# Performance work log

Hardware: AMD Instinct MI355X
Metric: run time of the kernel (lower is better)

The kernel has to match this reference:

```python
import jax, jax.numpy as jnp
import numpy as np

N = 50000       # nodes
E = 800000      # edges (avg degree 16)
IN = 256        # in_features
HEAD = 4        # attention heads (conv1/conv2 out_channels)
F_OUT = 32      # mlp output features per head


def setup_inputs() -> dict:
    key = jax.random.key(0)
    ks = jax.random.split(key, 6)
    feat = jax.random.normal(ks[0], (N, IN), dtype=jnp.float32)
    edge_index = jax.random.randint(ks[1], (2, E), 0, N, dtype=jnp.int64)
    s = 1.0 / np.sqrt(IN)
    # mlp: Linear(IN -> HEAD*F_OUT)
    W_mlp = jax.random.uniform(ks[2], (IN, HEAD * F_OUT), jnp.float32, -s, s)
    b_mlp = jnp.zeros((HEAD * F_OUT,), jnp.float32)
    # conv1/conv2: 1x1 Conv1d(IN -> HEAD) == linear projection
    W1 = jax.random.uniform(ks[3], (HEAD, IN), jnp.float32, -s, s)
    b1 = jnp.zeros((HEAD,), jnp.float32)
    W2 = jax.random.uniform(ks[4], (HEAD, IN), jnp.float32, -s, s)
    b2 = jnp.zeros((HEAD,), jnp.float32)
    eps = jnp.zeros((1,), jnp.float32)  # trainable eps, init 0
    return {"feat": feat, "edge_index": edge_index, "W_mlp": W_mlp,
            "b_mlp": b_mlp, "W1": W1, "b1": b1, "W2": W2, "b2": b2,
            "eps": eps}


def reference(feat, edge_index, W_mlp, b_mlp, W1, b1, W2, b2, eps):
    n = feat.shape[0]
    head = W1.shape[0]
    # mlp: [N, IN] -> [N, head*F] -> [head, N, F]
    x = (feat @ W_mlp + b_mlp).reshape(n, head, -1).transpose(1, 0, 2)
    # 1x1 conv projections -> per-node attention logits [head, N]
    h1 = (feat @ W1.T + b1).T
    h2 = (feat @ W2.T + b2).T
    src = edge_index[0]  # edge[0]
    dst = edge_index[1]  # edge[1]
    # per-edge attention value, relu (dropout=0 -> identity): [head, E]
    v = jax.nn.relu(h1[:, src] + h2[:, dst])
    # gather neighbor features and weight: [head, E, F]
    msg = x[:, dst, :] * v[:, :, None]
    # scatter-add into destination nodes indexed by src: [N, head, F]
    agg = jax.ops.segment_sum(msg.transpose(1, 0, 2), src, num_segments=n)
    h_prime = agg.transpose(1, 0, 2) + eps[0] * x   # [head, N, F]
    # permute(1,0,2).reshape(N, -1) -> [N, head*F]
    return h_prime.transpose(1, 0, 2).reshape(n, -1)
```

## Files before the change

### kernel.cpp

```cpp
#include <hip/hip_runtime.h>

#define NN   50000
#define EE   800000
#define INF  256
#define COUT 128
#define BTROWS 144
#define PROJ_BLOCKS 782
#define CAP  52

typedef __attribute__((ext_vector_type(8))) short short8;
typedef __attribute__((ext_vector_type(4))) float f32x4;

__device__ __forceinline__ float b2f(unsigned short u) {
    union { unsigned int i; float f; } c;
    c.i = ((unsigned int)u) << 16;
    return c.f;
}
__device__ __forceinline__ unsigned short f2b(float f) {
    union { float f; unsigned int i; } c;
    c.f = f;
    unsigned int i = c.i;
    unsigned int lsb = (i >> 16) & 1u;
    i += 0x7fffu + lsb;
    return (unsigned short)(i >> 16);
}

__global__ __launch_bounds__(256) void zero_bt_kernel(
    const float* __restrict__ Wm, const float* __restrict__ W1,
    const float* __restrict__ W2,
    unsigned short* __restrict__ BT, int* __restrict__ cursor)
{
    const int t = threadIdx.x;
    if (blockIdx.x < 49) {
        const int idx = blockIdx.x * 256 + t;
        if (idx < 12500) ((int4*)cursor)[idx] = make_int4(0, 0, 0, 0);
    } else {
        const int n = blockIdx.x - 49;
        const int k = t;
        float v;
        if      (n < 128) v = Wm[k * COUT + n];
        else if (n < 132) v = W1[(n - 128) * INF + k];
        else if (n < 136) v = W2[(n - 132) * INF + k];
        else              v = 0.f;
        BT[n * INF + k] = f2b(v);
    }
}

#define LSTRIDE 72
__global__ __launch_bounds__(256) void proj_scatter_kernel(
    const float* __restrict__ feat,
    const unsigned short* __restrict__ BT,
    const float* __restrict__ bm,
    const float* __restrict__ b1,
    const float* __restrict__ b2,
    unsigned short* __restrict__ x_out,
    unsigned short* __restrict__ hh,
    const int* __restrict__ edge,
    int* __restrict__ cursor,
    unsigned short* __restrict__ sdst)
{
    __shared__ short lA[64 * LSTRIDE];
    __shared__ short lB[BTROWS * LSTRIDE];

    const int t = threadIdx.x;

    if (blockIdx.x >= PROJ_BLOCKS) {
        const int e = (blockIdx.x - PROJ_BLOCKS) * 256 + t;
        const int s = edge[e];
        const int d = edge[EE + e];
        const int p = atomicAdd(&cursor[s], 1);
        if (p < CAP) sdst[s * CAP + p] = (unsigned short)d;
        return;
    }

    const int lane  = t & 63;
    const int wave  = t >> 6;
    const int quad  = lane >> 4;
    const int col   = lane & 15;
    const int node0 = blockIdx.x * 64;

    f32x4 acc[9];
    #pragma unroll
    for (int i = 0; i < 9; i++) acc[i] = (f32x4){0.f, 0.f, 0.f, 0.f};

    for (int kc = 0; kc < 4; kc++) {
        const int k0 = kc * 64;
        #pragma unroll
        for (int p = 0; p < 4; p++) {
            const int idx = p * 256 + t;
            const int row = idx >> 4;
            const int c4  = idx & 15;
            const int grow = node0 + row;
            float4 f = make_float4(0.f, 0.f, 0.f, 0.f);
            if (grow < NN) f = *(const float4*)(feat + grow * INF + k0 + c4 * 4);
            short4 s;
            s.x = (short)f2b(f.x); s.y = (short)f2b(f.y);
            s.z = (short)f2b(f.z); s.w = (short)f2b(f.w);
            *(short4*)&lA[row * LSTRIDE + c4 * 4] = s;
        }
        #pragma unroll
        for (int p = 0; p < 5; p++) {
            const int idx = p * 256 + t;
            if (idx < (BTROWS * 64) / 8) {
                const int row = idx >> 3;
                const int c8  = idx & 7;
                uint4 u = *(const uint4*)(BT + row * INF + k0 + c8 * 8);
                *(uint4*)&lB[row * LSTRIDE + c8 * 8] = u;
            }
        }
        __syncthreads();

        #pragma unroll
        for (int ks = 0; ks < 2; ks++) {
            short8 a = *(const short8*)&lA[(wave * 16 + col) * LSTRIDE + ks * 32 + quad * 8];
            #pragma unroll
            for (int nt = 0; nt < 9; nt++) {
                short8 b = *(const short8*)&lB[(nt * 16 + col) * LSTRIDE + ks * 32 + quad * 8];
                acc[nt] = __builtin_amdgcn_mfma_f32_16x16x32_bf16(a, b, acc[nt], 0, 0, 0);
            }
        }
        __syncthreads();
    }

    const int rbase = node0 + wave * 16 + quad * 4;
    #pragma unroll
    for (int nt = 0; nt < 8; nt++) {
        const float bias = bm[nt * 16 + col];
        #pragma unroll
        for (int r = 0; r < 4; r++) {
            const int row = rbase + r;
            if (row < NN) x_out[row * COUT + nt * 16 + col] = f2b(acc[nt][r] + bias);
        }
    }
    if (col < 8) {
        const float bias = (col < 4) ? b1[col] : b2[col - 4];
        #pragma unroll
        for (int r = 0; r < 4; r++) {
            const int row = rbase + r;
            if (row < NN) hh[row * 8 + col] = f2b(acc[8][r] + bias);
        }
    }
}

__global__ __launch_bounds__(256) void accum_kernel(
    const int* __restrict__ cursor,
    const unsigned short* __restrict__ sdst,
    const unsigned short* __restrict__ x,
    const unsigned short* __restrict__ hh,
    const float* __restrict__ eps,
    float* __restrict__ out)
{
    const int lane = threadIdx.x & 63;
    const int node = blockIdx.x * 4 + (threadIdx.x >> 6);
    if (node >= NN) return;

    const int sub = lane & 7;
    const int g   = lane >> 3;
    const int h   = sub >> 1;

    const int deg = min(cursor[node], CAP);

    ushort4 h1u = *(const ushort4*)(hh + node * 8);

    int dv = 0;
    unsigned int vv01 = 0, vv23 = 0;
    if (lane < deg) {
        dv = (int)sdst[node * CAP + lane];
        ushort4 h2u = *(const ushort4*)(hh + dv * 8 + 4);
        const float v0 = b2f(h1u.x) + b2f(h2u.x);
        const float v1 = b2f(h1u.y) + b2f(h2u.y);
        const float v2 = b2f(h1u.z) + b2f(h2u.z);
        const float v3 = b2f(h1u.w) + b2f(h2u.w);
        vv01 = (unsigned int)f2b(v0) | ((unsigned int)f2b(v1) << 16);
        vv23 = (unsigned int)f2b(v2) | ((unsigned int)f2b(v3) << 16);
    }

    float acc[16];
    #pragma unroll
    for (int r = 0; r < 16; r++) acc[r] = 0.f;

    for (int i0 = 0; i0 < deg; i0 += 8) {
        const int idx = i0 + g;
        const int d = __shfl(dv, idx);
        const unsigned int u01 = (unsigned int)__shfl((int)vv01, idx);
        const unsigned int u23 = (unsigned int)__shfl((int)vv23, idx);
        unsigned short vb;
        if      (h == 0) vb = (unsigned short)(u01 & 0xffffu);
        else if (h == 1) vb = (unsigned short)(u01 >> 16);
        else if (h == 2) vb = (unsigned short)(u23 & 0xffffu);
        else             vb = (unsigned short)(u23 >> 16);
        const float v = b2f(vb);
        if (idx < deg && v > 0.f) {
            const unsigned short* xr = x + d * COUT + sub * 16;
            uint4 u0 = *(const uint4*)(xr);
            uint4 u1 = *(const uint4*)(xr + 8);
            acc[0]  = fmaf(b2f((unsigned short)(u0.x & 0xffffu)), v, acc[0]);
            acc[1]  = fmaf(b2f((unsigned short)(u0.x >> 16)),     v, acc[1]);
            acc[2]  = fmaf(b2f((unsigned short)(u0.y & 0xffffu)), v, acc[2]);
            acc[3]  = fmaf(b2f((unsigned short)(u0.y >> 16)),     v, acc[3]);
            acc[4]  = fmaf(b2f((unsigned short)(u0.z & 0xffffu)), v, acc[4]);
            acc[5]  = fmaf(b2f((unsigned short)(u0.z >> 16)),     v, acc[5]);
            acc[6]  = fmaf(b2f((unsigned short)(u0.w & 0xffffu)), v, acc[6]);
            acc[7]  = fmaf(b2f((unsigned short)(u0.w >> 16)),     v, acc[7]);
            acc[8]  = fmaf(b2f((unsigned short)(u1.x & 0xffffu)), v, acc[8]);
            acc[9]  = fmaf(b2f((unsigned short)(u1.x >> 16)),     v, acc[9]);
            acc[10] = fmaf(b2f((unsigned short)(u1.y & 0xffffu)), v, acc[10]);
            acc[11] = fmaf(b2f((unsigned short)(u1.y >> 16)),     v, acc[11]);
            acc[12] = fmaf(b2f((unsigned short)(u1.z & 0xffffu)), v, acc[12]);
            acc[13] = fmaf(b2f((unsigned short)(u1.z >> 16)),     v, acc[13]);
            acc[14] = fmaf(b2f((unsigned short)(u1.w & 0xffffu)), v, acc[14]);
            acc[15] = fmaf(b2f((unsigned short)(u1.w >> 16)),     v, acc[15]);
        }
    }

    #pragma unroll
    for (int r = 0; r < 16; r++) {
        acc[r] += __shfl_xor(acc[r], 8);
        acc[r] += __shfl_xor(acc[r], 16);
        acc[r] += __shfl_xor(acc[r], 32);
    }

    if (lane < 8) {
        const float e = eps[0];
        const unsigned short* xr = x + node * COUT + sub * 16;
        uint4 u0 = *(const uint4*)(xr);
        uint4 u1 = *(const uint4*)(xr + 8);
        unsigned int uu[8] = {u0.x, u0.y, u0.z, u0.w, u1.x, u1.y, u1.z, u1.w};
        #pragma unroll
        for (int q = 0; q < 8; q++) {
            acc[2 * q]     = fmaf(e, b2f((unsigned short)(uu[q] & 0xffffu)), acc[2 * q]);
            acc[2 * q + 1] = fmaf(e, b2f((unsigned short)(uu[q] >> 16)),     acc[2 * q + 1]);
        }
        float* o = out + node * COUT + sub * 16;
        #pragma unroll
        for (int q = 0; q < 4; q++)
            *(float4*)(o + q * 4) = make_float4(acc[4 * q], acc[4 * q + 1],
                                                acc[4 * q + 2], acc[4 * q + 3]);
    }
}

extern "C" void kernel_launch(void* const* d_in, const int* in_sizes, int n_in,
                              void* d_out, int out_size, void* d_ws, size_t ws_size,
                              hipStream_t stream) {
    const float* feat = (const float*)d_in[0];
    const int*   edge = (const int*)d_in[1];
    const float* Wm   = (const float*)d_in[2];
    const float* bm   = (const float*)d_in[3];
    const float* W1   = (const float*)d_in[4];
    const float* b1   = (const float*)d_in[5];
    const float* W2   = (const float*)d_in[6];
    const float* b2   = (const float*)d_in[7];
    const float* eps  = (const float*)d_in[8];

    char* ws = (char*)d_ws;
    unsigned short* x      = (unsigned short*)ws;
    unsigned short* hh     = (unsigned short*)(ws + 12800000);
    int*            cursor = (int*)(ws + 13600000);
    unsigned short* sdst   = (unsigned short*)(ws + 13800000);
    unsigned short* BT     = (unsigned short*)d_out;

    zero_bt_kernel<<<193, 256, 0, stream>>>(Wm, W1, W2, BT, cursor);
    proj_scatter_kernel<<<PROJ_BLOCKS + 3125, 256, 0, stream>>>(
        feat, BT, bm, b1, b2, x, hh, edge, cursor, sdst);
    accum_kernel<<<(NN + 3) / 4, 256, 0, stream>>>(cursor, sdst, x, hh, eps,
                                                   (float*)d_out);
}
```

Measured before the change: 189.1 us.

## Replace per-node global atomics with two-level bucketed adjacency build in LDS

Edge scatter now bins edges into 196 buckets of 256 source nodes, using block-local LDS histograms and one global atomic per bucket per block instead of one global atomic per edge. A new kernel then builds each bucket's fixed-capacity adjacency lists in shared memory and writes them out as coalesced 8-byte stores along with the per-node counts. This is meant to cut global atomic contention and scattered 2-byte writes, at the cost of an extra kernel launch, an intermediate packed buffer placed in the output scratch area, and a per-bucket capacity limit of 4608 that could drop edges if a bucket overflows.

```diff
diff --git a/kernel.cpp b/kernel.cpp
--- a/kernel.cpp
+++ b/kernel.cpp
@@ -8,6 +8,11 @@
 #define PROJ_BLOCKS 782
 #define CAP  52
 
+#define NB   196
+#define BCAP 4608
+#define EPB  2048
+#define SC_BLOCKS ((EE + EPB - 1) / EPB)
+
 typedef __attribute__((ext_vector_type(8))) short short8;
 typedef __attribute__((ext_vector_type(4))) float f32x4;
 
@@ -28,14 +33,14 @@
 __global__ __launch_bounds__(256) void zero_bt_kernel(
     const float* __restrict__ Wm, const float* __restrict__ W1,
     const float* __restrict__ W2,
-    unsigned short* __restrict__ BT, int* __restrict__ cursor)
+    unsigned short* __restrict__ BT, int* __restrict__ bcnt)
 {
     const int t = threadIdx.x;
-    if (blockIdx.x < 49) {
-        const int idx = blockIdx.x * 256 + t;
-        if (idx < 12500) ((int4*)cursor)[idx] = make_int4(0, 0, 0, 0);
+    if (blockIdx.x == 0) {
+        #pragma unroll
+        for (int i = t; i < 784; i += 256) ((int4*)bcnt)[i] = make_int4(0, 0, 0, 0);
     } else {
-        const int n = blockIdx.x - 49;
+        const int n = blockIdx.x - 1;
         const int k = t;
         float v;
         if      (n < 128) v = Wm[k * COUT + n];
@@ -56,8 +61,8 @@
     unsigned short* __restrict__ x_out,
     unsigned short* __restrict__ hh,
     const int* __restrict__ edge,
-    int* __restrict__ cursor,
-    unsigned short* __restrict__ sdst)
+    int* __restrict__ bcnt,
+    unsigned int* __restrict__ bedges)
 {
     __shared__ short lA[64 * LSTRIDE];
     __shared__ short lB[BTROWS * LSTRIDE];
@@ -65,11 +70,37 @@
     const int t = threadIdx.x;
 
     if (blockIdx.x >= PROJ_BLOCKS) {
-        const int e = (blockIdx.x - PROJ_BLOCKS) * 256 + t;
-        const int s = edge[e];
-        const int d = edge[EE + e];
-        const int p = atomicAdd(&cursor[s], 1);
-        if (p < CAP) sdst[s * CAP + p] = (unsigned short)d;
+        int* lhist = (int*)lA;
+        int* lbase = lhist + 256;
+        if (t < NB) lhist[t] = 0;
+        __syncthreads();
+
+        const int e0 = (blockIdx.x - PROJ_BLOCKS) * EPB;
+        int s[8], d[8], pos[8];
+        #pragma unroll
+        for (int k = 0; k < 8; k++) {
+            const int e = e0 + k * 256 + t;
+            if (e < EE) {
+                s[k] = edge[e];
+                d[k] = edge[EE + e];
+                pos[k] = atomicAdd(&lhist[s[k] >> 8], 1);
+            } else {
+                pos[k] = -1;
+            }
+        }
+        __syncthreads();
+        if (t < NB) lbase[t] = atomicAdd(&bcnt[t * 16], lhist[t]);
+        __syncthreads();
+        #pragma unroll
+        for (int k = 0; k < 8; k++) {
+            if (pos[k] >= 0) {
+                const int b = s[k] >> 8;
+                const int p = lbase[b] + pos[k];
+                if (p < BCAP)
+                    bedges[b * BCAP + p] =
+                        ((unsigned int)(s[k] & 255) << 16) | (unsigned int)d[k];
+            }
+        }
         return;
     }
 
@@ -140,6 +171,37 @@
             if (row < NN) hh[row * 8 + col] = f2b(acc[8][r] + bias);
         }
     }
+}
+
+__global__ __launch_bounds__(256) void build_sdst_kernel(
+    const unsigned int* __restrict__ bedges,
+    const int* __restrict__ bcnt,
+    unsigned short* __restrict__ sdst,
+    int* __restrict__ cursor)
+{
+    __shared__ alignas(16) unsigned short ladj[256 * CAP];
+    __shared__ int lcur[256];
+    const int t = threadIdx.x;
+    const int b = blockIdx.x;
+    lcur[t] = 0;
+    __syncthreads();
+
+    const int cnt = min(bcnt[b * 16], BCAP);
+    for (int i = t; i < cnt; i += 256) {
+        const unsigned int pk = bedges[b * BCAP + i];
+        const int n = (int)(pk >> 16);
+        const int p = atomicAdd(&lcur[n], 1);
+        if (p < CAP) ladj[n * CAP + p] = (unsigned short)(pk & 0xffffu);
+    }
+    __syncthreads();
+
+    const int node0 = b << 8;
+    const int nvalid = min(256, NN - node0);
+    const int nu8 = nvalid * (CAP / 4);
+    unsigned long long* gs = (unsigned long long*)(sdst + (size_t)node0 * CAP);
+    const unsigned long long* ls = (const unsigned long long*)ladj;
+    for (int i = t; i < nu8; i += 256) gs[i] = ls[i];
+    if (t < nvalid) cursor[node0 + t] = min(lcur[t], CAP);
 }
 
 __global__ __launch_bounds__(256) void accum_kernel(
@@ -257,11 +319,15 @@
     unsigned short* hh     = (unsigned short*)(ws + 12800000);
     int*            cursor = (int*)(ws + 13600000);
     unsigned short* sdst   = (unsigned short*)(ws + 13800000);
+
     unsigned short* BT     = (unsigned short*)d_out;
-
-    zero_bt_kernel<<<193, 256, 0, stream>>>(Wm, W1, W2, BT, cursor);
-    proj_scatter_kernel<<<PROJ_BLOCKS + 3125, 256, 0, stream>>>(
-        feat, BT, bm, b1, b2, x, hh, edge, cursor, sdst);
+    int*            bcnt   = (int*)((char*)d_out + 131072);
+    unsigned int*   bedges = (unsigned int*)((char*)d_out + 262144);
+
+    zero_bt_kernel<<<145, 256, 0, stream>>>(Wm, W1, W2, BT, bcnt);
+    proj_scatter_kernel<<<PROJ_BLOCKS + SC_BLOCKS, 256, 0, stream>>>(
+        feat, BT, bm, b1, b2, x, hh, edge, bcnt, bedges);
+    build_sdst_kernel<<<NB, 256, 0, stream>>>(bedges, bcnt, sdst, cursor);
     accum_kernel<<<(NN + 3) / 4, 256, 0, stream>>>(cursor, sdst, x, hh, eps,
                                                    (float*)d_out);
 }
```

After: 174.2 us. 7.9% less time.
